# Optimization experiments

Hardware: AMD Instinct MI355X
Metric: run time of the kernel (lower is better)

## Reference

```python
import jax, jax.numpy as jnp
import numpy as np
import math

JOINT_DIM = 16
D_MODEL = 128
NUM_HEADS = 8
HEAD_DIM = D_MODEL // NUM_HEADS


def kinematic_adjacency():
    adj = np.zeros((JOINT_DIM, JOINT_DIM), dtype=np.float32)
    skeleton = [(0, 1), (1, 2), (2, 3), (0, 4), (4, 5), (5, 6), (0, 7), (7, 8),
                (8, 9), (0, 10), (10, 11), (11, 12), (0, 13), (13, 14), (14, 15)]
    for p, c in skeleton:
        adj[p, c] = 1.0
        adj[c, p] = 1.0
    sym = [(4, 7), (5, 8), (6, 9), (10, 13), (11, 14), (12, 15)]
    for a, b in sym:
        adj[a, b] += 0.8
        adj[b, a] += 0.8
    adj += np.eye(JOINT_DIM, dtype=np.float32)
    return jnp.asarray(adj)


def setup_inputs() -> dict:
    key = jax.random.key(0)
    ks = jax.random.split(key, 9)
    B, S = 64, 512
    s3 = 1.0 / math.sqrt(3.0)
    sd = 1.0 / math.sqrt(D_MODEL)
    return {
        "x": jax.random.normal(ks[0], (B, S, JOINT_DIM, 3), dtype=jnp.float32),
        "Wq": jax.random.uniform(ks[1], (3, D_MODEL), jnp.float32, -s3, s3),
        "bq": jax.random.uniform(ks[2], (D_MODEL,), jnp.float32, -s3, s3),
        "Wk": jax.random.uniform(ks[3], (3, D_MODEL), jnp.float32, -s3, s3),
        "bk": jax.random.uniform(ks[4], (D_MODEL,), jnp.float32, -s3, s3),
        "Wv": jax.random.uniform(ks[5], (3, D_MODEL), jnp.float32, -s3, s3),
        "bv": jax.random.uniform(ks[6], (D_MODEL,), jnp.float32, -s3, s3),
        "Wo": jax.random.uniform(ks[7], (D_MODEL, D_MODEL), jnp.float32, -sd, sd),
        "bo": jax.random.uniform(ks[8], (D_MODEL,), jnp.float32, -sd, sd),
    }


def reference(x, Wq, bq, Wk, bk, Wv, bv, Wo, bo):
    B, S, J, _ = x.shape
    adj = kinematic_adjacency()  # [J, J]

    def split_heads(t):  # [B,S,J,D] -> [B,S,H,J,hd]
        return t.reshape(B, S, J, NUM_HEADS, HEAD_DIM).transpose(0, 1, 3, 2, 4)

    q = split_heads(x @ Wq + bq)
    k = split_heads(x @ Wk + bk)
    v = split_heads(x @ Wv + bv)

    # scores get adjacency bias BEFORE the 1/sqrt(head_dim) scaling (as in source)
    scores = jnp.einsum('bshjd,bshkd->bshjk', q, k)
    scores = (scores + adj) / math.sqrt(HEAD_DIM)
    w = jax.nn.softmax(scores, axis=-1)  # dropout inactive (eval)
    ctx = jnp.einsum('bshjk,bshkd->bshjd', w, v)
    ctx = ctx.transpose(0, 1, 3, 2, 4).reshape(B, S, J, D_MODEL)
    return ctx @ Wo + bo  # [B,S,J,D]
```

## Files before the change

kernel.cpp:

```cpp
#include <hip/hip_runtime.h>

#define NJ   16
#define DM   128
#define NH   8
#define P    16
#define CL   0.36067376022224085f

typedef __attribute__((ext_vector_type(8))) short bf16x8;
typedef __attribute__((ext_vector_type(4))) float f32x4;
typedef __attribute__((ext_vector_type(2))) float f32x2;

__constant__ float c_adj[NJ * NJ] = {
    1,1,0,0, 1,0,0,1, 0,0,1,0, 0,1,0,0,
    1,1,1,0, 0,0,0,0, 0,0,0,0, 0,0,0,0,
    0,1,1,1, 0,0,0,0, 0,0,0,0, 0,0,0,0,
    0,0,1,1, 0,0,0,0, 0,0,0,0, 0,0,0,0,
    1,0,0,0, 1,1,0,0.8f, 0,0,0,0, 0,0,0,0,
    0,0,0,0, 1,1,1,0, 0.8f,0,0,0, 0,0,0,0,
    0,0,0,0, 0,1,1,0, 0,0.8f,0,0, 0,0,0,0,
    1,0,0,0, 0.8f,0,0,1, 1,0,0,0, 0,0,0,0,
    0,0,0,0, 0,0.8f,0,1, 1,1,0,0, 0,0,0,0,
    0,0,0,0, 0,0,0.8f,0, 1,1,0,0, 0,0,0,0,
    1,0,0,0, 0,0,0,0, 0,0,1,1, 0,0.8f,0,0,
    0,0,0,0, 0,0,0,0, 0,0,1,1, 1,0,0.8f,0,
    0,0,0,0, 0,0,0,0, 0,0,0,1, 1,0,0,0.8f,
    1,0,0,0, 0,0,0,0, 0,0,0.8f,0, 0,1,1,0,
    0,0,0,0, 0,0,0,0, 0,0,0,0.8f, 0,1,1,1,
    0,0,0,0, 0,0,0,0, 0,0,0,0, 0.8f,0,1,1
};

#define WS_BP_W   0
#define WS_PACK_W 128
#define WS_GF_W   256

__device__ __forceinline__ unsigned short f2bf(float f) {
    union { float f; unsigned u; } v; v.f = f;
    unsigned u = v.u;
    u += 0x7FFFu + ((u >> 16) & 1u);
    return (unsigned short)(u >> 16);
}
__device__ __forceinline__ unsigned pack2bf(float lo, float hi) {
    return (unsigned)f2bf(lo) | ((unsigned)f2bf(hi) << 16);
}

__global__ __launch_bounds__(256) void skel_setup_kernel(
    const float* __restrict__ Wq, const float* __restrict__ bq,
    const float* __restrict__ Wk, const float* __restrict__ bk,
    const float* __restrict__ Wv, const float* __restrict__ bv,
    const float* __restrict__ Wo, const float* __restrict__ bo,
    unsigned* __restrict__ wsu)
{
    const int b = blockIdx.x, t = threadIdx.x;
    float* wsf = (float*)wsu;

    if (b < 8) {
        const int idx = b * 256 + t;
        const int ctl = idx >> 2, i = idx & 3;
        const int ct = ctl >> 6, l = ctl & 63;
        const int n  = ct * 16 + (l & 15);
        const int kb = (l >> 4) * 8;
        float v[2];
#pragma unroll
        for (int s = 0; s < 2; ++s) {
            const int k = kb + 2 * i + s;
            const int h = k >> 2, r = k & 3;
            float acc = 0.f;
            if (r < 3) {
#pragma unroll
                for (int dh = 0; dh < 16; ++dh)
                    acc += Wv[r * DM + h * 16 + dh] * Wo[(h * 16 + dh) * DM + n];
            }
            v[s] = acc;
        }
        wsu[WS_GF_W + idx] = pack2bf(v[0], v[1]);
        return;
    }
    if (t < 128) {
        const int n = t;
        float bv_ = bo[n];
        for (int d = 0; d < DM; ++d) bv_ += bv[d] * Wo[d * DM + n];
        wsf[WS_BP_W + n] = bv_;
    } else if (t < 128 + NH) {
        const int h = t - 128;
        float* o = &wsf[WS_PACK_W + h * 16];
#pragma unroll
        for (int r = 0; r < 3; ++r)
#pragma unroll
            for (int c = 0; c < 3; ++c) {
                float acc = 0.f;
#pragma unroll
                for (int dh = 0; dh < 16; ++dh)
                    acc += Wq[r * DM + h * 16 + dh] * Wk[c * DM + h * 16 + dh];
                o[r * 3 + c] = acc * CL;
            }
#pragma unroll
        for (int r = 0; r < 3; ++r) {
            float aa = 0.f, cc = 0.f;
#pragma unroll
            for (int dh = 0; dh < 16; ++dh) {
                aa += Wq[r * DM + h * 16 + dh] * bk[h * 16 + dh];
                cc += Wk[r * DM + h * 16 + dh] * bq[h * 16 + dh];
            }
            o[9 + r]  = aa * CL;
            o[12 + r] = cc * CL;
        }
        float dd = 0.f;
#pragma unroll
        for (int dh = 0; dh < 16; ++dh) dd += bq[h * 16 + dh] * bk[h * 16 + dh];
        o[15] = dd * CL;
    }
}

__global__ __launch_bounds__(256) void skel_main_kernel(
    const float* __restrict__ x,
    const unsigned* __restrict__ wsu,
    float* __restrict__ out,
    int npos)
{
    const int t = threadIdx.x;
    const long pos0 = (long)blockIdx.x * P;
    const float* wsf = (const float*)wsu;

    __shared__ __align__(16) float    sx4[P][NJ][4];
    __shared__ float                  sc[128];
    __shared__ __align__(16) float    sbp[128];
    __shared__ __align__(16) float    sout[4][NJ * DM];

    {
        const int p = t >> 4, j = t & 15;
        const long pidx = pos0 + p;
        const long base = pidx * 48 + j * 3;
        const bool ok = pidx < npos;
        sx4[p][j][0] = ok ? x[base + 0] : 0.f;
        sx4[p][j][1] = ok ? x[base + 1] : 0.f;
        sx4[p][j][2] = ok ? x[base + 2] : 0.f;
        sx4[p][j][3] = 0.f;
    }
    if (t < 128) sc[t]        = wsf[WS_PACK_W + t];
    else         sbp[t - 128] = wsf[WS_BP_W + (t - 128)];
    const int l = t & 63;
    bf16x8 ga[8];
#pragma unroll
    for (int ct = 0; ct < 8; ++ct)
        ga[ct] = *(const bf16x8*)&wsu[WS_GF_W + (ct * 64 + l) * 4];
    __syncthreads();

    const int wv = t >> 6;
    const int h  = l >> 3, j0 = l & 7;
    const int jB = l & 15, lkB = l >> 4;

    float m[16];
#pragma unroll
    for (int i = 0; i < 16; ++i) m[i] = sc[h * 16 + i];
    f32x2 adjp[NJ];
#pragma unroll
    for (int k = 0; k < NJ; ++k) {
        adjp[k].x = c_adj[j0 * NJ + k] * CL;
        adjp[k].y = c_adj[(j0 + 8) * NJ + k] * CL;
    }

    float*    so   = &sout[wv][0];
    unsigned* sxbw = (unsigned*)&sout[wv][NJ * DM - 320];

    for (int it = 0; it < 4; ++it) {
        const int p = wv * 4 + it;
        const f32x4 xa = *(const f32x4*)&sx4[p][j0];
        const f32x4 xb = *(const f32x4*)&sx4[p][j0 + 8];
        const f32x2 px = { xa.x, xb.x };
        const f32x2 py = { xa.y, xb.y };
        const f32x2 pz = { xa.z, xb.z };

        const f32x2 y0 = m[0]*px + m[3]*py + m[6]*pz + m[12];
        const f32x2 y1 = m[1]*px + m[4]*py + m[7]*pz + m[13];
        const f32x2 y2 = m[2]*px + m[5]*py + m[8]*pz + m[14];
        const f32x2 uu = m[9]*px + m[10]*py + m[11]*pz + m[15];

        f32x2 sum = { 0.f, 0.f };
        f32x2 A0 = { 0.f, 0.f }, A1 = { 0.f, 0.f }, A2 = { 0.f, 0.f };
#pragma unroll
        for (int k = 0; k < NJ; ++k) {
            const f32x4 xk = *(const f32x4*)&sx4[p][k];
            const f32x2 s = y0 * xk.x + y1 * xk.y + y2 * xk.z + (uu + adjp[k]);
            f32x2 e;
            e.x = exp2f(s.x);
            e.y = exp2f(s.y);
            sum += e;
            A0 += e * xk.x;
            A1 += e * xk.y;
            A2 += e * xk.z;
        }
        f32x2 inv;
        inv.x = __builtin_amdgcn_rcpf(sum.x);
        inv.y = __builtin_amdgcn_rcpf(sum.y);
        const f32x2 b0 = A0 * inv, b1 = A1 * inv, b2 = A2 * inv;

        {
            uint2 w0, w1;
            w0.x = pack2bf(b0.x, b1.x);
            w0.y = pack2bf(b2.x, 0.f);
            w1.x = pack2bf(b0.y, b1.y);
            w1.y = pack2bf(b2.y, 0.f);
            *(uint2*)&sxbw[j0 * 20 + 2 * h]       = w0;
            *(uint2*)&sxbw[(j0 + 8) * 20 + 2 * h] = w1;
        }
        const bf16x8 bvec = *(const bf16x8*)&sxbw[jB * 20 + lkB * 4];

        __builtin_amdgcn_s_setprio(1);
#pragma unroll
        for (int ct = 0; ct < 8; ++ct) {
            f32x4 acc = *(const f32x4*)&sbp[ct * 16 + lkB * 4];
            acc = __builtin_amdgcn_mfma_f32_16x16x32_bf16(ga[ct], bvec, acc, 0, 0, 0);
            *(f32x4*)&so[jB * 128 + (((ct * 4 + lkB) ^ (jB & 7)) << 2)] = acc;
        }
        __builtin_amdgcn_s_setprio(0);

        if (pos0 + p < npos) {
            float* ob = out + (pos0 + p) * (long)(NJ * DM);
#pragma unroll
            for (int c2 = 0; c2 < 8; ++c2) {
                const int jR = c2 * 2 + (l >> 5);
                const int ul = l & 31;
                const f32x4 vq = *(const f32x4*)&so[jR * 128 + ((ul ^ (jR & 7)) << 2)];
                *(f32x4*)(ob + c2 * 256 + l * 4) = vq;
            }
        }
    }
}

extern "C" void kernel_launch(void* const* d_in, const int* in_sizes, int n_in,
                              void* d_out, int out_size, void* d_ws, size_t ws_size,
                              hipStream_t stream) {
    const float* x  = (const float*)d_in[0];
    const float* Wq = (const float*)d_in[1];
    const float* bq = (const float*)d_in[2];
    const float* Wk = (const float*)d_in[3];
    const float* bk = (const float*)d_in[4];
    const float* Wv = (const float*)d_in[5];
    const float* bv = (const float*)d_in[6];
    const float* Wo = (const float*)d_in[7];
    const float* bo = (const float*)d_in[8];
    float* out    = (float*)d_out;
    unsigned* wsu = (unsigned*)d_ws;

    const int npos = in_sizes[0] / (NJ * 3);
    skel_setup_kernel<<<9, 256, 0, stream>>>(Wq, bq, Wk, bk, Wv, bv, Wo, bo, wsu);
    const int grid = (npos + P - 1) / P;
    skel_main_kernel<<<grid, 256, 0, stream>>>(x, wsu, out, npos);
}
```

Before: 64.18 us.

## Specialize waves into compute and store roles with double-buffered output staging

Each block now handles 128 positions with 512 threads: four waves compute attention and the MFMA projection into a double-buffered LDS staging area, while four other waves stream the previous round's results to global memory. This aims to overlap the heavy output stores with compute and amortize setup loads over more positions. In exchange it adds a block-wide barrier every round, uses more LDS, and shrinks the grid to far fewer, larger blocks, which may lower occupancy and memory-level parallelism.

```diff
diff --git a/kernel.cpp b/kernel.cpp
--- a/kernel.cpp
+++ b/kernel.cpp
@@ -3,7 +3,9 @@
 #define NJ   16
 #define DM   128
 #define NH   8
-#define P    16
+#define PPB  128
+#define NW_C 4
+#define ROUNDS (PPB / NW_C)
 #define CL   0.36067376022224085f
 
 typedef __attribute__((ext_vector_type(8))) short bf16x8;
@@ -111,119 +113,130 @@
     }
 }
 
-__global__ __launch_bounds__(256) void skel_main_kernel(
+__global__ __launch_bounds__(512) void skel_main_kernel(
     const float* __restrict__ x,
     const unsigned* __restrict__ wsu,
     float* __restrict__ out,
     int npos)
 {
     const int t = threadIdx.x;
-    const long pos0 = (long)blockIdx.x * P;
+    const int wv = t >> 6, l = t & 63;
     const float* wsf = (const float*)wsu;
-
-    __shared__ __align__(16) float    sx4[P][NJ][4];
+    const long base = (long)blockIdx.x * PPB;
+
+    __shared__ __align__(16) float    sx4[PPB][NJ][4];
     __shared__ float                  sc[128];
     __shared__ __align__(16) float    sbp[128];
-    __shared__ __align__(16) float    sout[4][NJ * DM];
+    __shared__ __align__(16) unsigned sxb[NW_C][NJ * 20];
+    __shared__ __align__(16) float    sout[2][NW_C][NJ * DM];
 
     {
-        const int p = t >> 4, j = t & 15;
-        const long pidx = pos0 + p;
-        const long base = pidx * 48 + j * 3;
-        const bool ok = pidx < npos;
-        sx4[p][j][0] = ok ? x[base + 0] : 0.f;
-        sx4[p][j][1] = ok ? x[base + 1] : 0.f;
-        sx4[p][j][2] = ok ? x[base + 2] : 0.f;
-        sx4[p][j][3] = 0.f;
-    }
-    if (t < 128) sc[t]        = wsf[WS_PACK_W + t];
-    else         sbp[t - 128] = wsf[WS_BP_W + (t - 128)];
-    const int l = t & 63;
+        const long lim = (long)npos * 48;
+        for (int i = t; i < PPB * 48; i += 512) {
+            const long gi = base * 48 + i;
+            const int e = i % 48;
+            sx4[i / 48][e / 3][e % 3] = (gi < lim) ? x[gi] : 0.f;
+        }
+    }
+    if (t < 128)      sc[t]        = wsf[WS_PACK_W + t];
+    else if (t < 256) sbp[t - 128] = wsf[WS_BP_W + (t - 128)];
+
     bf16x8 ga[8];
 #pragma unroll
     for (int ct = 0; ct < 8; ++ct)
         ga[ct] = *(const bf16x8*)&wsu[WS_GF_W + (ct * 64 + l) * 4];
     __syncthreads();
 
-    const int wv = t >> 6;
     const int h  = l >> 3, j0 = l & 7;
     const int jB = l & 15, lkB = l >> 4;
 
     float m[16];
-#pragma unroll
-    for (int i = 0; i < 16; ++i) m[i] = sc[h * 16 + i];
     f32x2 adjp[NJ];
-#pragma unroll
-    for (int k = 0; k < NJ; ++k) {
-        adjp[k].x = c_adj[j0 * NJ + k] * CL;
-        adjp[k].y = c_adj[(j0 + 8) * NJ + k] * CL;
-    }
-
-    float*    so   = &sout[wv][0];
-    unsigned* sxbw = (unsigned*)&sout[wv][NJ * DM - 320];
-
-    for (int it = 0; it < 4; ++it) {
-        const int p = wv * 4 + it;
-        const f32x4 xa = *(const f32x4*)&sx4[p][j0];
-        const f32x4 xb = *(const f32x4*)&sx4[p][j0 + 8];
-        const f32x2 px = { xa.x, xb.x };
-        const f32x2 py = { xa.y, xb.y };
-        const f32x2 pz = { xa.z, xb.z };
-
-        const f32x2 y0 = m[0]*px + m[3]*py + m[6]*pz + m[12];
-        const f32x2 y1 = m[1]*px + m[4]*py + m[7]*pz + m[13];
-        const f32x2 y2 = m[2]*px + m[5]*py + m[8]*pz + m[14];
-        const f32x2 uu = m[9]*px + m[10]*py + m[11]*pz + m[15];
-
-        f32x2 sum = { 0.f, 0.f };
-        f32x2 A0 = { 0.f, 0.f }, A1 = { 0.f, 0.f }, A2 = { 0.f, 0.f };
+    if (wv < NW_C) {
+#pragma unroll
+        for (int i = 0; i < 16; ++i) m[i] = sc[h * 16 + i];
 #pragma unroll
         for (int k = 0; k < NJ; ++k) {
-            const f32x4 xk = *(const f32x4*)&sx4[p][k];
-            const f32x2 s = y0 * xk.x + y1 * xk.y + y2 * xk.z + (uu + adjp[k]);
-            f32x2 e;
-            e.x = exp2f(s.x);
-            e.y = exp2f(s.y);
-            sum += e;
-            A0 += e * xk.x;
-            A1 += e * xk.y;
-            A2 += e * xk.z;
-        }
-        f32x2 inv;
-        inv.x = __builtin_amdgcn_rcpf(sum.x);
-        inv.y = __builtin_amdgcn_rcpf(sum.y);
-        const f32x2 b0 = A0 * inv, b1 = A1 * inv, b2 = A2 * inv;
-
-        {
-            uint2 w0, w1;
-            w0.x = pack2bf(b0.x, b1.x);
-            w0.y = pack2bf(b2.x, 0.f);
-            w1.x = pack2bf(b0.y, b1.y);
-            w1.y = pack2bf(b2.y, 0.f);
-            *(uint2*)&sxbw[j0 * 20 + 2 * h]       = w0;
-            *(uint2*)&sxbw[(j0 + 8) * 20 + 2 * h] = w1;
-        }
-        const bf16x8 bvec = *(const bf16x8*)&sxbw[jB * 20 + lkB * 4];
-
-        __builtin_amdgcn_s_setprio(1);
-#pragma unroll
-        for (int ct = 0; ct < 8; ++ct) {
-            f32x4 acc = *(const f32x4*)&sbp[ct * 16 + lkB * 4];
-            acc = __builtin_amdgcn_mfma_f32_16x16x32_bf16(ga[ct], bvec, acc, 0, 0, 0);
-            *(f32x4*)&so[jB * 128 + (((ct * 4 + lkB) ^ (jB & 7)) << 2)] = acc;
-        }
-        __builtin_amdgcn_s_setprio(0);
-
-        if (pos0 + p < npos) {
-            float* ob = out + (pos0 + p) * (long)(NJ * DM);
-#pragma unroll
-            for (int c2 = 0; c2 < 8; ++c2) {
-                const int jR = c2 * 2 + (l >> 5);
-                const int ul = l & 31;
-                const f32x4 vq = *(const f32x4*)&so[jR * 128 + ((ul ^ (jR & 7)) << 2)];
-                *(f32x4*)(ob + c2 * 256 + l * 4) = vq;
-            }
-        }
+            adjp[k].x = c_adj[j0 * NJ + k] * CL;
+            adjp[k].y = c_adj[(j0 + 8) * NJ + k] * CL;
+        }
+    }
+
+    for (int r = 0; r <= ROUNDS; ++r) {
+        if (wv < NW_C) {
+            if (r < ROUNDS) {
+                const int p = r * NW_C + wv;
+                if (base + p < npos) {
+                    const f32x4 xa = *(const f32x4*)&sx4[p][j0];
+                    const f32x4 xb = *(const f32x4*)&sx4[p][j0 + 8];
+                    const f32x2 px = { xa.x, xb.x };
+                    const f32x2 py = { xa.y, xb.y };
+                    const f32x2 pz = { xa.z, xb.z };
+
+                    const f32x2 y0 = m[0]*px + m[3]*py + m[6]*pz + m[12];
+                    const f32x2 y1 = m[1]*px + m[4]*py + m[7]*pz + m[13];
+                    const f32x2 y2 = m[2]*px + m[5]*py + m[8]*pz + m[14];
+                    const f32x2 uu = m[9]*px + m[10]*py + m[11]*pz + m[15];
+
+                    f32x2 sum = { 0.f, 0.f };
+                    f32x2 A0 = { 0.f, 0.f }, A1 = { 0.f, 0.f }, A2 = { 0.f, 0.f };
+#pragma unroll
+                    for (int k = 0; k < NJ; ++k) {
+                        const f32x4 xk = *(const f32x4*)&sx4[p][k];
+                        const f32x2 sv = y0*xk.x + y1*xk.y + y2*xk.z + (uu + adjp[k]);
+                        f32x2 e;
+                        e.x = exp2f(sv.x);
+                        e.y = exp2f(sv.y);
+                        sum += e;
+                        A0 += e * xk.x;
+                        A1 += e * xk.y;
+                        A2 += e * xk.z;
+                    }
+                    f32x2 inv;
+                    inv.x = __builtin_amdgcn_rcpf(sum.x);
+                    inv.y = __builtin_amdgcn_rcpf(sum.y);
+                    const f32x2 b0 = A0 * inv, b1 = A1 * inv, b2 = A2 * inv;
+
+                    unsigned* sxbw = &sxb[wv][0];
+                    {
+                        uint2 w0, w1;
+                        w0.x = pack2bf(b0.x, b1.x);
+                        w0.y = pack2bf(b2.x, 0.f);
+                        w1.x = pack2bf(b0.y, b1.y);
+                        w1.y = pack2bf(b2.y, 0.f);
+                        *(uint2*)&sxbw[j0 * 20 + 2 * h]       = w0;
+                        *(uint2*)&sxbw[(j0 + 8) * 20 + 2 * h] = w1;
+                    }
+                    const bf16x8 bvec = *(const bf16x8*)&sxbw[jB * 20 + lkB * 4];
+
+                    float* sb = &sout[r & 1][wv][0];
+                    __builtin_amdgcn_s_setprio(1);
+#pragma unroll
+                    for (int ct = 0; ct < 8; ++ct) {
+                        f32x4 acc = *(const f32x4*)&sbp[ct * 16 + lkB * 4];
+                        acc = __builtin_amdgcn_mfma_f32_16x16x32_bf16(ga[ct], bvec, acc, 0, 0, 0);
+                        *(f32x4*)&sb[jB * 128 + (((ct * 4 + lkB) ^ (jB & 7)) << 2)] = acc;
+                    }
+                    __builtin_amdgcn_s_setprio(0);
+                }
+            }
+        } else {
+            if (r >= 1) {
+                const int p = (r - 1) * NW_C + (wv - NW_C);
+                if (base + p < npos) {
+                    const float* sb = &sout[(r - 1) & 1][wv - NW_C][0];
+                    float* ob = out + (base + p) * (long)(NJ * DM);
+#pragma unroll
+                    for (int c2 = 0; c2 < 8; ++c2) {
+                        const int jR = c2 * 2 + (l >> 5);
+                        const int ul = l & 31;
+                        const f32x4 vq = *(const f32x4*)&sb[jR * 128 + ((ul ^ (jR & 7)) << 2)];
+                        *(f32x4*)(ob + c2 * 256 + l * 4) = vq;
+                    }
+                }
+            }
+        }
+        __syncthreads();
     }
 }
 
@@ -244,6 +257,6 @@
 
     const int npos = in_sizes[0] / (NJ * 3);
     skel_setup_kernel<<<9, 256, 0, stream>>>(Wq, bq, Wk, bk, Wv, bv, Wo, bo, wsu);
-    const int grid = (npos + P - 1) / P;
-    skel_main_kernel<<<grid, 256, 0, stream>>>(x, wsu, out, npos);
-}
+    const int grid = (npos + PPB - 1) / PPB;
+    skel_main_kernel<<<grid, 512, 0, stream>>>(x, wsu, out, npos);
+}
```

New measurement: 68.69 us. 1.07x slower.
